# Kernel tuning notes

Hardware: AMD Instinct MI355X
Metric: run time of the kernel (lower is better)

## Reference

```python
import jax, jax.numpy as jnp
import numpy as np

B, DIM, W = 16, 128, 16384
HEADS, DIM_HEAD = 4, 32
HIDDEN = HEADS * DIM_HEAD  # 128
SCALE = DIM_HEAD ** -0.5
EPS = 1e-5


def setup_inputs() -> dict:
    key = jax.random.key(0)
    k0, k1, k2, k3 = jax.random.split(key, 4)
    x = jax.random.normal(k0, (B, DIM, W), dtype=jnp.float32)
    # pointwise Conv1d weights (kernel_size=1) stored as [out_ch, in_ch]
    W_qkv = jax.random.normal(k1, (HIDDEN * 3, DIM), dtype=jnp.float32) * 0.02
    W_out = jax.random.normal(k2, (DIM, HIDDEN), dtype=jnp.float32) * 0.02
    b_out = jnp.zeros((DIM,), dtype=jnp.float32)
    gamma = jnp.ones((DIM,), dtype=jnp.float32)
    beta = jnp.zeros((DIM,), dtype=jnp.float32)
    return {"x": x, "W_qkv": W_qkv, "W_out": W_out, "b_out": b_out,
            "gamma": gamma, "beta": beta}


def reference(x, W_qkv, W_out, b_out, gamma, beta):
    b, c, w = x.shape
    # pointwise conv = channel matmul: (3*hidden, c) @ (b, c, w) -> (b, 3*hidden, w)
    qkv = jnp.einsum('oc,bcw->bow', W_qkv, x)
    q, k, v = jnp.split(qkv, 3, axis=1)
    rs = lambda t: t.reshape(b, HEADS, DIM_HEAD, w)  # b (h d) w -> b h d w
    q, k, v = rs(q), rs(k), rs(v)
    q = jax.nn.softmax(q, axis=-2) * SCALE   # softmax over head-dim d
    k = jax.nn.softmax(k, axis=-1)           # softmax over length n
    v = v / w
    # context: (b h d e) = sum_n k[b h d n] v[b h e n]
    context = jnp.einsum('bhdn,bhen->bhde', k, v)
    out = jnp.einsum('bhde,bhdn->bhen', context, q)  # (b h e n)
    out = out.reshape(b, HIDDEN, w)
    y = jnp.einsum('oc,bcw->bow', W_out, out) + b_out[None, :, None]
    # channel-wise LayerNorm over dim=1 (biased variance)
    mean = jnp.mean(y, axis=1, keepdims=True)
    var = jnp.var(y, axis=1, keepdims=True)
    y = (y - mean) * jax.lax.rsqrt(var + EPS)
    return y * gamma[None, :, None] + beta[None, :, None]
```

## Files before the change

### kernel.cpp

```cpp
#include <hip/hip_runtime.h>
#include <cstddef>

#define WLEN 16384
#define SCALEQ 0.17677669529663687f
#define CB_SCALE 16777216.0f
#define CB_INV   5.9604644775390625e-08f

typedef _Float16 half8 __attribute__((ext_vector_type(8)));
typedef _Float16 half4 __attribute__((ext_vector_type(4)));
typedef _Float16 half2v __attribute__((ext_vector_type(2)));
typedef float float4v __attribute__((ext_vector_type(4)));

#define WS_CTX 0
#define WS_DEN 65536
#define WS_WH  67584
#define WS_CB  92160

#define MFMA16(a, b, c) __builtin_amdgcn_mfma_f32_16x16x32_f16(a, b, c, 0, 0, 0)

__global__ __launch_bounds__(256) void k0_prep(const float* __restrict__ Wqkv,
                                               float* __restrict__ ws) {
  int idx = blockIdx.x * 256 + threadIdx.x;
  _Float16* Wh = (_Float16*)(ws + WS_WH);
  if (idx < 49152) Wh[idx] = (_Float16)Wqkv[idx];
}

__global__ __launch_bounds__(256, 2) void ka_ctx(
    const float* __restrict__ x, float* __restrict__ ws) {
  __shared__ __align__(16) _Float16 xh[32 * 136];
  __shared__ __align__(16) _Float16 ekl[4 * 32 * 40];
  __shared__ __align__(16) _Float16 vl[4 * 32 * 40];
  const int tid = threadIdx.x;
  const int lane = tid & 63, wv = tid >> 6;
  const int l15 = lane & 15, quad = lane >> 4;
  const int b = blockIdx.y, chunk = blockIdx.x;
  const _Float16* Wh = (const _Float16*)(ws + WS_WH);
  float* ctx = ws + WS_CTX;
  float* den = ws + WS_DEN;
  const float* xb = x + (size_t)b * 128 * WLEN;

  half8 afr[4][4];
  #pragma unroll
  for (int mt = 0; mt < 4; ++mt) {
    int row = (mt < 2) ? (128 + 32 * wv + mt * 16 + l15)
                       : (256 + 32 * wv + (mt - 2) * 16 + l15);
    #pragma unroll
    for (int ks = 0; ks < 4; ++ks)
      afr[mt][ks] = *(const half8*)(Wh + row * 128 + ks * 32 + quad * 8);
  }

  const float4v zero4 = {0.f, 0.f, 0.f, 0.f};
  float4v ctxa[2][2] = {zero4, zero4, zero4, zero4};
  float denr[8] = {0.f, 0.f, 0.f, 0.f, 0.f, 0.f, 0.f, 0.f};

  for (int s = 0; s < 16; ++s) {
    const int n0 = chunk * 512 + s * 32;
    __syncthreads();
    #pragma unroll
    for (int it = 0; it < 2; ++it) {
      int idx = it * 256 + tid;
      int f = idx & 7, cp = idx >> 3;
      const float* p0 = xb + (size_t)(2 * cp) * WLEN + n0 + 4 * f;
      float4 a = *(const float4*)p0;
      float4 c = *(const float4*)(p0 + WLEN);
      float av[4] = {a.x, a.y, a.z, a.w};
      float cv[4] = {c.x, c.y, c.z, c.w};
      #pragma unroll
      for (int i = 0; i < 4; ++i) {
        half2v h; h[0] = (_Float16)av[i]; h[1] = (_Float16)cv[i];
        *(half2v*)&xh[(4 * f + i) * 136 + 2 * cp] = h;
      }
    }
    __syncthreads();
    float4v acc[4][2] = {zero4, zero4, zero4, zero4, zero4, zero4, zero4, zero4};
    #pragma unroll
    for (int ks = 0; ks < 4; ++ks) {
      half8 b0 = *(const half8*)&xh[l15 * 136 + ks * 32 + quad * 8];
      half8 b1 = *(const half8*)&xh[(16 + l15) * 136 + ks * 32 + quad * 8];
      #pragma unroll
      for (int mt = 0; mt < 4; ++mt) {
        acc[mt][0] = MFMA16(afr[mt][ks], b0, acc[mt][0]);
        acc[mt][1] = MFMA16(afr[mt][ks], b1, acc[mt][1]);
      }
    }
    #pragma unroll
    for (int mt = 0; mt < 2; ++mt)
      #pragma unroll
      for (int nt = 0; nt < 2; ++nt)
        #pragma unroll
        for (int r = 0; r < 4; ++r) {
          float e = __expf(acc[mt][nt][r]);
          denr[mt * 4 + r] += e;
          ekl[(wv * 32 + mt * 16 + quad * 4 + r) * 40 + nt * 16 + l15] = (_Float16)e;
        }
    #pragma unroll
    for (int mt = 0; mt < 2; ++mt)
      #pragma unroll
      for (int nt = 0; nt < 2; ++nt)
        #pragma unroll
        for (int r = 0; r < 4; ++r)
          vl[(wv * 32 + mt * 16 + quad * 4 + r) * 40 + nt * 16 + l15] =
              (_Float16)acc[mt + 2][nt][r];
    half8 ae0 = *(const half8*)&ekl[(wv * 32 + l15) * 40 + quad * 8];
    half8 ae1 = *(const half8*)&ekl[(wv * 32 + 16 + l15) * 40 + quad * 8];
    half8 bv0 = *(const half8*)&vl[(wv * 32 + l15) * 40 + quad * 8];
    half8 bv1 = *(const half8*)&vl[(wv * 32 + 16 + l15) * 40 + quad * 8];
    ctxa[0][0] = MFMA16(ae0, bv0, ctxa[0][0]);
    ctxa[0][1] = MFMA16(ae0, bv1, ctxa[0][1]);
    ctxa[1][0] = MFMA16(ae1, bv0, ctxa[1][0]);
    ctxa[1][1] = MFMA16(ae1, bv1, ctxa[1][1]);
  }
  #pragma unroll
  for (int dt = 0; dt < 2; ++dt)
    #pragma unroll
    for (int et = 0; et < 2; ++et)
      #pragma unroll
      for (int r = 0; r < 4; ++r)
        atomicAdd(&ctx[((b * 4 + wv) * 32 + dt * 16 + quad * 4 + r) * 32 +
                       et * 16 + l15],
                  ctxa[dt][et][r]);
  #pragma unroll
  for (int i = 0; i < 8; ++i) {
    float v = denr[i];
    v += __shfl_xor(v, 1, 64);
    v += __shfl_xor(v, 2, 64);
    v += __shfl_xor(v, 4, 64);
    v += __shfl_xor(v, 8, 64);
    if (l15 == 0)
      atomicAdd(&den[(b * 4 + wv) * 32 + (i >> 2) * 16 + quad * 4 + (i & 3)], v);
  }
}

__global__ __launch_bounds__(256) void kb_cb(
    const float* __restrict__ Wout, float* __restrict__ ws) {
  __shared__ __align__(16) float nc[4096];
  const int b = blockIdx.x, tid = threadIdx.x;
  const float* ctx = ws + WS_CTX;
  const float* den = ws + WS_DEN;
  _Float16* cb = (_Float16*)(ws + WS_CB) + b * 16384;
  for (int i = tid; i < 4096; i += 256)
    nc[i] = ctx[b * 4096 + i] / (den[b * 128 + (i >> 5)] * 16384.0f);
  __syncthreads();
  const int o = tid >> 1, dh = (tid & 1) * 16;
  for (int h = 0; h < 4; ++h) {
    float wrow[32];
    #pragma unroll
    for (int e4 = 0; e4 < 8; ++e4) {
      float4 w4 = *(const float4*)(Wout + o * 128 + h * 32 + e4 * 4);
      wrow[e4 * 4 + 0] = w4.x; wrow[e4 * 4 + 1] = w4.y;
      wrow[e4 * 4 + 2] = w4.z; wrow[e4 * 4 + 3] = w4.w;
    }
    for (int d = 0; d < 16; ++d) {
      const float* ncr = &nc[(h * 32 + dh + d) * 32];
      float acc = 0.f;
      #pragma unroll
      for (int e = 0; e < 32; ++e) acc += wrow[e] * ncr[e];
      cb[o * 128 + h * 32 + dh + d] = (_Float16)(acc * CB_SCALE);
    }
  }
}

__global__ __launch_bounds__(256, 2) void kc_out(
    const float* __restrict__ x, const float* __restrict__ wsc,
    const float* __restrict__ b_out, const float* __restrict__ gamma,
    const float* __restrict__ beta, float* __restrict__ out) {
  __shared__ __align__(16) _Float16 xh[128 * 136];
  __shared__ float ssum[4][128], ssq[4][128];
  __shared__ float smean[128], sinv[128];
  const int tid = threadIdx.x;
  const int lane = tid & 63, wv = tid >> 6;
  const int l15 = lane & 15, quad = lane >> 4;
  const int b = blockIdx.y, tile = blockIdx.x;
  const int n0 = tile * 128;
  const _Float16* Wh = (const _Float16*)(wsc + WS_WH);
  const _Float16* cb = (const _Float16*)(wsc + WS_CB) + b * 16384;
  const float* xb = x + (size_t)b * 128 * WLEN;
  const float4v zero4 = {0.f, 0.f, 0.f, 0.f};

  half8 a1[2][4];
  #pragma unroll
  for (int mt = 0; mt < 2; ++mt)
    #pragma unroll
    for (int ks = 0; ks < 4; ++ks)
      a1[mt][ks] = *(const half8*)(Wh + (32 * wv + mt * 16 + l15) * 128 +
                                   ks * 32 + quad * 8);

  #pragma unroll
  for (int it = 0; it < 8; ++it) {
    int idx = it * 256 + tid;
    int f = (idx & 7) | ((idx >> 9) << 3);
    int cp = (idx >> 3) & 63;
    const float* p0 = xb + (size_t)(2 * cp) * WLEN + n0 + 4 * f;
    float4 a = *(const float4*)p0;
    float4 c = *(const float4*)(p0 + WLEN);
    float av[4] = {a.x, a.y, a.z, a.w};
    float cv[4] = {c.x, c.y, c.z, c.w};
    #pragma unroll
    for (int i = 0; i < 4; ++i) {
      half2v h; h[0] = (_Float16)av[i]; h[1] = (_Float16)cv[i];
      *(half2v*)&xh[(4 * f + i) * 136 + 2 * cp] = h;
    }
  }
  __syncthreads();

  float4v acc[2][8] = {zero4, zero4, zero4, zero4, zero4, zero4, zero4, zero4,
                       zero4, zero4, zero4, zero4, zero4, zero4, zero4, zero4};
  #pragma unroll
  for (int ks = 0; ks < 4; ++ks) {
    half8 bf[8];
    #pragma unroll
    for (int nt = 0; nt < 8; ++nt)
      bf[nt] = *(const half8*)&xh[(nt * 16 + l15) * 136 + ks * 32 + quad * 8];
    #pragma unroll
    for (int mt = 0; mt < 2; ++mt)
      #pragma unroll
      for (int nt = 0; nt < 8; ++nt)
        acc[mt][nt] = MFMA16(a1[mt][ks], bf[nt], acc[mt][nt]);
  }
  #pragma unroll
  for (int nt = 0; nt < 8; ++nt) {
    float mx = -1e30f;
    #pragma unroll
    for (int mt = 0; mt < 2; ++mt)
      #pragma unroll
      for (int r = 0; r < 4; ++r) mx = fmaxf(mx, acc[mt][nt][r]);
    mx = fmaxf(mx, __shfl_xor(mx, 16, 64));
    mx = fmaxf(mx, __shfl_xor(mx, 32, 64));
    float sm = 0.f;
    #pragma unroll
    for (int mt = 0; mt < 2; ++mt)
      #pragma unroll
      for (int r = 0; r < 4; ++r) {
        float e = __expf(acc[mt][nt][r] - mx);
        acc[mt][nt][r] = e;
        sm += e;
      }
    sm += __shfl_xor(sm, 16, 64);
    sm += __shfl_xor(sm, 32, 64);
    float sc = SCALEQ / sm;
    #pragma unroll
    for (int mt = 0; mt < 2; ++mt)
      #pragma unroll
      for (int r = 0; r < 4; ++r) acc[mt][nt][r] *= sc;
  }
  __syncthreads();
  #pragma unroll
  for (int mt = 0; mt < 2; ++mt)
    #pragma unroll
    for (int nt = 0; nt < 8; ++nt) {
      half4 hq;
      #pragma unroll
      for (int r = 0; r < 4; ++r) hq[r] = (_Float16)acc[mt][nt][r];
      *(half4*)&xh[(nt * 16 + l15) * 136 + 32 * wv + mt * 16 + quad * 4] = hq;
    }
  __syncthreads();

  half8 a2[2][4];
  #pragma unroll
  for (int mt = 0; mt < 2; ++mt)
    #pragma unroll
    for (int ks = 0; ks < 4; ++ks)
      a2[mt][ks] = *(const half8*)(cb + (32 * wv + mt * 16 + l15) * 128 +
                                   ks * 32 + quad * 8);
  float4v acc2[2][8] = {zero4, zero4, zero4, zero4, zero4, zero4, zero4, zero4,
                        zero4, zero4, zero4, zero4, zero4, zero4, zero4, zero4};
  #pragma unroll
  for (int ks = 0; ks < 4; ++ks) {
    half8 bf[8];
    #pragma unroll
    for (int nt = 0; nt < 8; ++nt)
      bf[nt] = *(const half8*)&xh[(nt * 16 + l15) * 136 + ks * 32 + quad * 8];
    #pragma unroll
    for (int mt = 0; mt < 2; ++mt)
      #pragma unroll
      for (int nt = 0; nt < 8; ++nt)
        acc2[mt][nt] = MFMA16(a2[mt][ks], bf[nt], acc2[mt][nt]);
  }

  float bo[8], ga[8], be[8];
  #pragma unroll
  for (int mt = 0; mt < 2; ++mt)
    #pragma unroll
    for (int r = 0; r < 4; ++r) {
      int o = 32 * wv + mt * 16 + quad * 4 + r;
      bo[mt * 4 + r] = b_out[o];
      ga[mt * 4 + r] = gamma[o];
      be[mt * 4 + r] = beta[o];
    }
  #pragma unroll
  for (int nt = 0; nt < 8; ++nt) {
    float ps = 0.f, pq = 0.f;
    #pragma unroll
    for (int mt = 0; mt < 2; ++mt)
      #pragma unroll
      for (int r = 0; r < 4; ++r) {
        float v = acc2[mt][nt][r] * CB_INV + bo[mt * 4 + r];
        acc2[mt][nt][r] = v;
        ps += v;
        pq += v * v;
      }
    ps += __shfl_xor(ps, 16, 64);
    ps += __shfl_xor(ps, 32, 64);
    pq += __shfl_xor(pq, 16, 64);
    pq += __shfl_xor(pq, 32, 64);
    if (quad == 0) {
      ssum[wv][nt * 16 + l15] = ps;
      ssq[wv][nt * 16 + l15] = pq;
    }
  }
  __syncthreads();
  if (tid < 128) {
    float s = ssum[0][tid] + ssum[1][tid] + ssum[2][tid] + ssum[3][tid];
    float q2 = ssq[0][tid] + ssq[1][tid] + ssq[2][tid] + ssq[3][tid];
    float mean = s * (1.0f / 128.0f);
    float var = q2 * (1.0f / 128.0f) - mean * mean;
    smean[tid] = mean;
    sinv[tid] = rsqrtf(var + 1e-5f);
  }
  __syncthreads();
  float* ob = out + (size_t)b * 128 * WLEN + n0;
  #pragma unroll
  for (int nt = 0; nt < 8; ++nt) {
    int n = nt * 16 + l15;
    float mean = smean[n], inv = sinv[n];
    #pragma unroll
    for (int mt = 0; mt < 2; ++mt)
      #pragma unroll
      for (int r = 0; r < 4; ++r) {
        int o = 32 * wv + mt * 16 + quad * 4 + r;
        ob[(size_t)o * WLEN + n] =
            (acc2[mt][nt][r] - mean) * inv * ga[mt * 4 + r] + be[mt * 4 + r];
      }
  }
}

extern "C" void kernel_launch(void* const* d_in, const int* in_sizes, int n_in,
                              void* d_out, int out_size, void* d_ws, size_t ws_size,
                              hipStream_t stream) {
  const float* x    = (const float*)d_in[0];
  const float* Wqkv = (const float*)d_in[1];
  const float* Wout = (const float*)d_in[2];
  const float* bo   = (const float*)d_in[3];
  const float* gam  = (const float*)d_in[4];
  const float* bet  = (const float*)d_in[5];
  float* out = (float*)d_out;
  float* ws  = (float*)d_ws;

  hipMemsetAsync(ws, 0, (65536 + 2048) * sizeof(float), stream);
  hipLaunchKernelGGL(k0_prep, dim3(192), dim3(256), 0, stream, Wqkv, ws);
  hipLaunchKernelGGL(ka_ctx, dim3(32, 16), dim3(256), 0, stream, x, ws);
  hipLaunchKernelGGL(kb_cb, dim3(16), dim3(256), 0, stream, Wout, ws);
  hipLaunchKernelGGL(kc_out, dim3(128, 16), dim3(256), 0, stream,
                     x, ws, bo, gam, bet, out);
}
```

Before: 304.7 us.

## Transpose MFMA operand roles so outputs vectorize and LayerNorm reduces in-wave

In the context kernel, x tiles become the MFMA A operand and the W_qkv rows the B operand. The step widens to 64 positions, and exp/v values are written to LDS as half4 vectors, so the inner context MFMA runs two k-steps. In the output kernel, the second GEMM swaps operands so each lane holds 4 consecutive positions for one output channel. This allows float4 stores to global memory and a LayerNorm reduction done entirely with wave shuffles, removing shared-memory reductions and two barriers. The x loads now read 4 channels per thread and write half4 to LDS. The cost is more register pressure and larger LDS footprints.

```diff
diff --git a/kernel.cpp b/kernel.cpp
--- a/kernel.cpp
+++ b/kernel.cpp
@@ -8,7 +8,6 @@
 
 typedef _Float16 half8 __attribute__((ext_vector_type(8)));
 typedef _Float16 half4 __attribute__((ext_vector_type(4)));
-typedef _Float16 half2v __attribute__((ext_vector_type(2)));
 typedef float float4v __attribute__((ext_vector_type(4)));
 
 #define WS_CTX 0
@@ -27,9 +26,9 @@
 
 __global__ __launch_bounds__(256, 2) void ka_ctx(
     const float* __restrict__ x, float* __restrict__ ws) {
-  __shared__ __align__(16) _Float16 xh[32 * 136];
-  __shared__ __align__(16) _Float16 ekl[4 * 32 * 40];
-  __shared__ __align__(16) _Float16 vl[4 * 32 * 40];
+  __shared__ __align__(16) _Float16 xh[64 * 136];
+  __shared__ __align__(16) _Float16 ekl[4][32 * 72];
+  __shared__ __align__(16) _Float16 vl[4][32 * 72];
   const int tid = threadIdx.x;
   const int lane = tid & 63, wv = tid >> 6;
   const int l15 = lane & 15, quad = lane >> 4;
@@ -39,76 +38,96 @@
   float* den = ws + WS_DEN;
   const float* xb = x + (size_t)b * 128 * WLEN;
 
-  half8 afr[4][4];
-  #pragma unroll
-  for (int mt = 0; mt < 4; ++mt) {
-    int row = (mt < 2) ? (128 + 32 * wv + mt * 16 + l15)
-                       : (256 + 32 * wv + (mt - 2) * 16 + l15);
+  half8 bw[4][4];
+  #pragma unroll
+  for (int nt = 0; nt < 4; ++nt) {
+    int row = (nt < 2) ? (128 + 32 * wv + nt * 16 + l15)
+                       : (256 + 32 * wv + (nt - 2) * 16 + l15);
     #pragma unroll
     for (int ks = 0; ks < 4; ++ks)
-      afr[mt][ks] = *(const half8*)(Wh + row * 128 + ks * 32 + quad * 8);
+      bw[nt][ks] = *(const half8*)(Wh + row * 128 + ks * 32 + quad * 8);
   }
 
   const float4v zero4 = {0.f, 0.f, 0.f, 0.f};
   float4v ctxa[2][2] = {zero4, zero4, zero4, zero4};
-  float denr[8] = {0.f, 0.f, 0.f, 0.f, 0.f, 0.f, 0.f, 0.f};
-
-  for (int s = 0; s < 16; ++s) {
-    const int n0 = chunk * 512 + s * 32;
+  float denr[2] = {0.f, 0.f};
+  const int f = tid & 7, cq = tid >> 3;
+
+  for (int s = 0; s < 8; ++s) {
+    const int n0 = chunk * 512 + s * 64;
     __syncthreads();
     #pragma unroll
     for (int it = 0; it < 2; ++it) {
-      int idx = it * 256 + tid;
-      int f = idx & 7, cp = idx >> 3;
-      const float* p0 = xb + (size_t)(2 * cp) * WLEN + n0 + 4 * f;
-      float4 a = *(const float4*)p0;
-      float4 c = *(const float4*)(p0 + WLEN);
-      float av[4] = {a.x, a.y, a.z, a.w};
-      float cv[4] = {c.x, c.y, c.z, c.w};
+      const int nn = it * 32 + 4 * f;
+      const float* p = xb + (size_t)(4 * cq) * WLEN + n0 + nn;
+      float4 r0 = *(const float4*)(p);
+      float4 r1 = *(const float4*)(p + WLEN);
+      float4 r2 = *(const float4*)(p + 2 * WLEN);
+      float4 r3 = *(const float4*)(p + 3 * WLEN);
+      float c0[4] = {r0.x, r0.y, r0.z, r0.w};
+      float c1[4] = {r1.x, r1.y, r1.z, r1.w};
+      float c2[4] = {r2.x, r2.y, r2.z, r2.w};
+      float c3[4] = {r3.x, r3.y, r3.z, r3.w};
       #pragma unroll
       for (int i = 0; i < 4; ++i) {
-        half2v h; h[0] = (_Float16)av[i]; h[1] = (_Float16)cv[i];
-        *(half2v*)&xh[(4 * f + i) * 136 + 2 * cp] = h;
+        half4 h;
+        h[0] = (_Float16)c0[i]; h[1] = (_Float16)c1[i];
+        h[2] = (_Float16)c2[i]; h[3] = (_Float16)c3[i];
+        *(half4*)&xh[(nn + i) * 136 + 4 * cq] = h;
       }
     }
     __syncthreads();
-    float4v acc[4][2] = {zero4, zero4, zero4, zero4, zero4, zero4, zero4, zero4};
+    float4v acc[4][4] = {zero4, zero4, zero4, zero4, zero4, zero4, zero4, zero4,
+                         zero4, zero4, zero4, zero4, zero4, zero4, zero4, zero4};
     #pragma unroll
     for (int ks = 0; ks < 4; ++ks) {
-      half8 b0 = *(const half8*)&xh[l15 * 136 + ks * 32 + quad * 8];
-      half8 b1 = *(const half8*)&xh[(16 + l15) * 136 + ks * 32 + quad * 8];
+      half8 af[4];
+      #pragma unroll
+      for (int mt = 0; mt < 4; ++mt)
+        af[mt] = *(const half8*)&xh[(mt * 16 + l15) * 136 + ks * 32 + quad * 8];
+      #pragma unroll
+      for (int mt = 0; mt < 4; ++mt)
+        #pragma unroll
+        for (int nt = 0; nt < 4; ++nt)
+          acc[mt][nt] = MFMA16(af[mt], bw[nt][ks], acc[mt][nt]);
+    }
+    #pragma unroll
+    for (int nt = 0; nt < 2; ++nt)
       #pragma unroll
       for (int mt = 0; mt < 4; ++mt) {
-        acc[mt][0] = MFMA16(afr[mt][ks], b0, acc[mt][0]);
-        acc[mt][1] = MFMA16(afr[mt][ks], b1, acc[mt][1]);
-      }
-    }
-    #pragma unroll
-    for (int mt = 0; mt < 2; ++mt)
-      #pragma unroll
-      for (int nt = 0; nt < 2; ++nt)
+        half4 h;
         #pragma unroll
         for (int r = 0; r < 4; ++r) {
           float e = __expf(acc[mt][nt][r]);
-          denr[mt * 4 + r] += e;
-          ekl[(wv * 32 + mt * 16 + quad * 4 + r) * 40 + nt * 16 + l15] = (_Float16)e;
+          denr[nt] += e;
+          h[r] = (_Float16)e;
         }
-    #pragma unroll
-    for (int mt = 0; mt < 2; ++mt)
-      #pragma unroll
-      for (int nt = 0; nt < 2; ++nt)
+        *(half4*)&ekl[wv][(nt * 16 + l15) * 72 + mt * 16 + quad * 4] = h;
+      }
+    #pragma unroll
+    for (int et = 0; et < 2; ++et)
+      #pragma unroll
+      for (int mt = 0; mt < 4; ++mt) {
+        half4 h;
         #pragma unroll
-        for (int r = 0; r < 4; ++r)
-          vl[(wv * 32 + mt * 16 + quad * 4 + r) * 40 + nt * 16 + l15] =
-              (_Float16)acc[mt + 2][nt][r];
-    half8 ae0 = *(const half8*)&ekl[(wv * 32 + l15) * 40 + quad * 8];
-    half8 ae1 = *(const half8*)&ekl[(wv * 32 + 16 + l15) * 40 + quad * 8];
-    half8 bv0 = *(const half8*)&vl[(wv * 32 + l15) * 40 + quad * 8];
-    half8 bv1 = *(const half8*)&vl[(wv * 32 + 16 + l15) * 40 + quad * 8];
-    ctxa[0][0] = MFMA16(ae0, bv0, ctxa[0][0]);
-    ctxa[0][1] = MFMA16(ae0, bv1, ctxa[0][1]);
-    ctxa[1][0] = MFMA16(ae1, bv0, ctxa[1][0]);
-    ctxa[1][1] = MFMA16(ae1, bv1, ctxa[1][1]);
+        for (int r = 0; r < 4; ++r) h[r] = (_Float16)acc[mt][et + 2][r];
+        *(half4*)&vl[wv][(et * 16 + l15) * 72 + mt * 16 + quad * 4] = h;
+      }
+    #pragma unroll
+    for (int ks = 0; ks < 2; ++ks) {
+      half8 ae[2], bv[2];
+      #pragma unroll
+      for (int dt = 0; dt < 2; ++dt)
+        ae[dt] = *(const half8*)&ekl[wv][(dt * 16 + l15) * 72 + ks * 32 + quad * 8];
+      #pragma unroll
+      for (int et = 0; et < 2; ++et)
+        bv[et] = *(const half8*)&vl[wv][(et * 16 + l15) * 72 + ks * 32 + quad * 8];
+      #pragma unroll
+      for (int dt = 0; dt < 2; ++dt)
+        #pragma unroll
+        for (int et = 0; et < 2; ++et)
+          ctxa[dt][et] = MFMA16(ae[dt], bv[et], ctxa[dt][et]);
+    }
   }
   #pragma unroll
   for (int dt = 0; dt < 2; ++dt)
@@ -120,14 +139,11 @@
                        et * 16 + l15],
                   ctxa[dt][et][r]);
   #pragma unroll
-  for (int i = 0; i < 8; ++i) {
-    float v = denr[i];
-    v += __shfl_xor(v, 1, 64);
-    v += __shfl_xor(v, 2, 64);
-    v += __shfl_xor(v, 4, 64);
-    v += __shfl_xor(v, 8, 64);
-    if (l15 == 0)
-      atomicAdd(&den[(b * 4 + wv) * 32 + (i >> 2) * 16 + quad * 4 + (i & 3)], v);
+  for (int nt = 0; nt < 2; ++nt) {
+    float v = denr[nt];
+    v += __shfl_xor(v, 16, 64);
+    v += __shfl_xor(v, 32, 64);
+    if (quad == 0) atomicAdd(&den[(b * 4 + wv) * 32 + nt * 16 + l15], v);
   }
 }
 
@@ -165,15 +181,13 @@
     const float* __restrict__ b_out, const float* __restrict__ gamma,
     const float* __restrict__ beta, float* __restrict__ out) {
   __shared__ __align__(16) _Float16 xh[128 * 136];
-  __shared__ float ssum[4][128], ssq[4][128];
-  __shared__ float smean[128], sinv[128];
   const int tid = threadIdx.x;
   const int lane = tid & 63, wv = tid >> 6;
   const int l15 = lane & 15, quad = lane >> 4;
   const int b = blockIdx.y, tile = blockIdx.x;
   const int n0 = tile * 128;
   const _Float16* Wh = (const _Float16*)(wsc + WS_WH);
-  const _Float16* cb = (const _Float16*)(wsc + WS_CB) + b * 16384;
+  const _Float16* cbg = (const _Float16*)(wsc + WS_CB) + b * 16384;
   const float* xb = x + (size_t)b * 128 * WLEN;
   const float4v zero4 = {0.f, 0.f, 0.f, 0.f};
 
@@ -185,20 +199,25 @@
       a1[mt][ks] = *(const half8*)(Wh + (32 * wv + mt * 16 + l15) * 128 +
                                    ks * 32 + quad * 8);
 
-  #pragma unroll
-  for (int it = 0; it < 8; ++it) {
-    int idx = it * 256 + tid;
-    int f = (idx & 7) | ((idx >> 9) << 3);
-    int cp = (idx >> 3) & 63;
-    const float* p0 = xb + (size_t)(2 * cp) * WLEN + n0 + 4 * f;
-    float4 a = *(const float4*)p0;
-    float4 c = *(const float4*)(p0 + WLEN);
-    float av[4] = {a.x, a.y, a.z, a.w};
-    float cv[4] = {c.x, c.y, c.z, c.w};
+  const int f = tid & 7, cq = tid >> 3;
+  #pragma unroll
+  for (int it = 0; it < 4; ++it) {
+    const int nn = it * 32 + 4 * f;
+    const float* p = xb + (size_t)(4 * cq) * WLEN + n0 + nn;
+    float4 r0 = *(const float4*)(p);
+    float4 r1 = *(const float4*)(p + WLEN);
+    float4 r2 = *(const float4*)(p + 2 * WLEN);
+    float4 r3 = *(const float4*)(p + 3 * WLEN);
+    float c0[4] = {r0.x, r0.y, r0.z, r0.w};
+    float c1[4] = {r1.x, r1.y, r1.z, r1.w};
+    float c2[4] = {r2.x, r2.y, r2.z, r2.w};
+    float c3[4] = {r3.x, r3.y, r3.z, r3.w};
     #pragma unroll
     for (int i = 0; i < 4; ++i) {
-      half2v h; h[0] = (_Float16)av[i]; h[1] = (_Float16)cv[i];
-      *(half2v*)&xh[(4 * f + i) * 136 + 2 * cp] = h;
+      half4 h;
+      h[0] = (_Float16)c0[i]; h[1] = (_Float16)c1[i];
+      h[2] = (_Float16)c2[i]; h[3] = (_Float16)c3[i];
+      *(half4*)&xh[(nn + i) * 136 + 4 * cq] = h;
     }
   }
   __syncthreads();
@@ -255,83 +274,75 @@
     }
   __syncthreads();
 
-  half8 a2[2][4];
-  #pragma unroll
-  for (int mt = 0; mt < 2; ++mt)
-    #pragma unroll
-    for (int ks = 0; ks < 4; ++ks)
-      a2[mt][ks] = *(const half8*)(cb + (32 * wv + mt * 16 + l15) * 128 +
-                                   ks * 32 + quad * 8);
   float4v acc2[2][8] = {zero4, zero4, zero4, zero4, zero4, zero4, zero4, zero4,
                         zero4, zero4, zero4, zero4, zero4, zero4, zero4, zero4};
   #pragma unroll
   for (int ks = 0; ks < 4; ++ks) {
-    half8 bf[8];
+    half8 aq[2];
+    #pragma unroll
+    for (int mt = 0; mt < 2; ++mt)
+      aq[mt] = *(const half8*)&xh[(32 * wv + mt * 16 + l15) * 136 +
+                                  ks * 32 + quad * 8];
+    half8 bc[8];
     #pragma unroll
     for (int nt = 0; nt < 8; ++nt)
-      bf[nt] = *(const half8*)&xh[(nt * 16 + l15) * 136 + ks * 32 + quad * 8];
+      bc[nt] = *(const half8*)(cbg + (nt * 16 + l15) * 128 + ks * 32 + quad * 8);
     #pragma unroll
     for (int mt = 0; mt < 2; ++mt)
       #pragma unroll
       for (int nt = 0; nt < 8; ++nt)
-        acc2[mt][nt] = MFMA16(a2[mt][ks], bf[nt], acc2[mt][nt]);
+        acc2[mt][nt] = MFMA16(aq[mt], bc[nt], acc2[mt][nt]);
   }
 
   float bo[8], ga[8], be[8];
   #pragma unroll
+  for (int nt = 0; nt < 8; ++nt) {
+    int o = nt * 16 + l15;
+    bo[nt] = b_out[o];
+    ga[nt] = gamma[o];
+    be[nt] = beta[o];
+  }
+  #pragma unroll
+  for (int mt = 0; mt < 2; ++mt)
+    #pragma unroll
+    for (int nt = 0; nt < 8; ++nt)
+      #pragma unroll
+      for (int r = 0; r < 4; ++r)
+        acc2[mt][nt][r] = acc2[mt][nt][r] * CB_INV + bo[nt];
+  float meanr[2][4], invr[2][4];
+  #pragma unroll
   for (int mt = 0; mt < 2; ++mt)
     #pragma unroll
     for (int r = 0; r < 4; ++r) {
-      int o = 32 * wv + mt * 16 + quad * 4 + r;
-      bo[mt * 4 + r] = b_out[o];
-      ga[mt * 4 + r] = gamma[o];
-      be[mt * 4 + r] = beta[o];
-    }
-  #pragma unroll
-  for (int nt = 0; nt < 8; ++nt) {
-    float ps = 0.f, pq = 0.f;
-    #pragma unroll
-    for (int mt = 0; mt < 2; ++mt)
-      #pragma unroll
-      for (int r = 0; r < 4; ++r) {
-        float v = acc2[mt][nt][r] * CB_INV + bo[mt * 4 + r];
-        acc2[mt][nt][r] = v;
+      float ps = 0.f, pq = 0.f;
+      #pragma unroll
+      for (int nt = 0; nt < 8; ++nt) {
+        float v = acc2[mt][nt][r];
         ps += v;
         pq += v * v;
       }
-    ps += __shfl_xor(ps, 16, 64);
-    ps += __shfl_xor(ps, 32, 64);
-    pq += __shfl_xor(pq, 16, 64);
-    pq += __shfl_xor(pq, 32, 64);
-    if (quad == 0) {
-      ssum[wv][nt * 16 + l15] = ps;
-      ssq[wv][nt * 16 + l15] = pq;
-    }
-  }
-  __syncthreads();
-  if (tid < 128) {
-    float s = ssum[0][tid] + ssum[1][tid] + ssum[2][tid] + ssum[3][tid];
-    float q2 = ssq[0][tid] + ssq[1][tid] + ssq[2][tid] + ssq[3][tid];
-    float mean = s * (1.0f / 128.0f);
-    float var = q2 * (1.0f / 128.0f) - mean * mean;
-    smean[tid] = mean;
-    sinv[tid] = rsqrtf(var + 1e-5f);
-  }
-  __syncthreads();
+      ps += __shfl_xor(ps, 1, 64); pq += __shfl_xor(pq, 1, 64);
+      ps += __shfl_xor(ps, 2, 64); pq += __shfl_xor(pq, 2, 64);
+      ps += __shfl_xor(ps, 4, 64); pq += __shfl_xor(pq, 4, 64);
+      ps += __shfl_xor(ps, 8, 64); pq += __shfl_xor(pq, 8, 64);
+      float mean = ps * (1.0f / 128.0f);
+      float var = pq * (1.0f / 128.0f) - mean * mean;
+      meanr[mt][r] = mean;
+      invr[mt][r] = rsqrtf(var + 1e-5f);
+    }
   float* ob = out + (size_t)b * 128 * WLEN + n0;
   #pragma unroll
-  for (int nt = 0; nt < 8; ++nt) {
-    int n = nt * 16 + l15;
-    float mean = smean[n], inv = sinv[n];
-    #pragma unroll
-    for (int mt = 0; mt < 2; ++mt)
-      #pragma unroll
-      for (int r = 0; r < 4; ++r) {
-        int o = 32 * wv + mt * 16 + quad * 4 + r;
-        ob[(size_t)o * WLEN + n] =
-            (acc2[mt][nt][r] - mean) * inv * ga[mt * 4 + r] + be[mt * 4 + r];
-      }
-  }
+  for (int mt = 0; mt < 2; ++mt)
+    #pragma unroll
+    for (int nt = 0; nt < 8; ++nt) {
+      float4 o4;
+      o4.x = (acc2[mt][nt][0] - meanr[mt][0]) * invr[mt][0] * ga[nt] + be[nt];
+      o4.y = (acc2[mt][nt][1] - meanr[mt][1]) * invr[mt][1] * ga[nt] + be[nt];
+      o4.z = (acc2[mt][nt][2] - meanr[mt][2]) * invr[mt][2] * ga[nt] + be[nt];
+      o4.w = (acc2[mt][nt][3] - meanr[mt][3]) * invr[mt][3] * ga[nt] + be[nt];
+      *(float4*)(ob + (size_t)(nt * 16 + l15) * WLEN + 32 * wv + mt * 16 +
+                 quad * 4) = o4;
+    }
 }
 
 extern "C" void kernel_launch(void* const* d_in, const int* in_sizes, int n_in,
```

Measured after the change: 332.5 us. 9.1% more time.
